# Kernel tuning notes

Measured on AMD Instinct MI355X. Metric: run time of the kernel, lower is better.

The kernel has to match this reference:

```python
import jax, jax.numpy as jnp
import numpy as np

T, N, F_IND, F_MAC = 250, 4000, 46, 178
H = 64
F_IN = F_IND + F_MAC  # dense-net input = firm chars + tiled macro = 224


def setup_inputs() -> dict:
    key = jax.random.key(0)
    ks = jax.random.split(key, 9)
    macro_features = jax.random.normal(ks[0], (1, T, F_MAC), jnp.float32)
    individual_features = jax.random.normal(ks[1], (1, T, N, F_IND), jnp.float32)
    masks = jnp.ones((1, T, N, 1), dtype=bool)
    returns_tensor = jax.random.normal(ks[2], (1, T, N, 1), jnp.float32) * 0.05
    W1 = jax.random.normal(ks[3], (F_IN, H), jnp.float32) / np.sqrt(F_IN).astype(np.float32)
    b1 = jnp.zeros((H,), jnp.float32)
    W2 = jax.random.normal(ks[4], (H, H), jnp.float32) / np.sqrt(H).astype(np.float32)
    b2 = jnp.zeros((H,), jnp.float32)
    W3 = jax.random.normal(ks[5], (H, 1), jnp.float32) / np.sqrt(H).astype(np.float32)
    b3 = jnp.zeros((1,), jnp.float32)
    return {"macro_features": macro_features, "individual_features": individual_features,
            "masks": masks, "returns_tensor": returns_tensor,
            "W1": W1, "b1": b1, "W2": W2, "b2": b2, "W3": W3, "b3": b3}


def reference(macro_features, individual_features, masks, returns_tensor, W1, b1, W2, b2, W3, b3):
    B, Tt, Nn, _ = individual_features.shape
    # tile macro state over assets and concat with firm characteristics -> [1,T,N,F_IN]
    mac = jnp.broadcast_to(macro_features[:, :, None, :], (B, Tt, Nn, macro_features.shape[-1]))
    dense_inputs = jnp.concatenate([individual_features, mac], axis=-1)
    mf = masks.astype(dense_inputs.dtype)  # [1,T,N,1]
    # dense net: 2 relu hidden layers + linear head, output_size=1 (SDF weight per firm-month)
    h = jax.nn.relu(dense_inputs @ W1 + b1)
    h = jax.nn.relu(h @ W2 + b2)
    weights = (h @ W3 + b3) * mf  # zero out masked entries (mask is all-ones -> static shape)
    # weighted returns and per-time segment sum (== torch.split + per-segment torch.sum)
    weighted_returns = returns_tensor * weights * mf
    num_val_per_time = jnp.sum(mf[0, :, :, 0], axis=1)  # [T]
    sum_per_time = jnp.sum(weighted_returns[0, :, :, 0], axis=1)  # [T]
    # normalize_w = True
    sum_per_time = sum_per_time / num_val_per_time * jnp.mean(num_val_per_time)
    sdf = (sum_per_time + 1.0)[:, None]  # [T,1]
    weights_flat = weights.reshape(1, Tt * Nn, 1)  # matches masked_select layout (all-true mask)
    return sdf, weights_flat
```

## Files before the change

kernel.cpp:

```cpp
#include <hip/hip_runtime.h>

#define T_DIM 250
#define N_DIM 4000
#define F_IND 46
#define F_MAC 178
#define H_DIM 64

typedef __bf16         bf16x8  __attribute__((ext_vector_type(8)));
typedef float          f32x4   __attribute__((ext_vector_type(4)));
typedef unsigned short ushort8 __attribute__((ext_vector_type(8)));
typedef float          f32x4a8 __attribute__((ext_vector_type(4), aligned(8)));

union FragU { ushort8 u; bf16x8 b; };
union BF2   { unsigned u; __bf16 h[2]; };

__device__ __forceinline__ unsigned short f2bf(float f) {
    unsigned u = __float_as_uint(f);
    return (unsigned short)((u + 0x7fffu + ((u >> 16) & 1u)) >> 16);
}
__device__ __forceinline__ unsigned packbf2(float lo, float hi) {
    BF2 p; p.h[0] = (__bf16)lo; p.h[1] = (__bf16)hi; return p.u;
}

__global__ __launch_bounds__(256)
void prep_kernel(const float* __restrict__ mac,
                 const float* __restrict__ W1,
                 const float* __restrict__ b1,
                 const float* __restrict__ W2,
                 unsigned short* __restrict__ Wb1,
                 unsigned short* __restrict__ Wb2,
                 float* __restrict__ Mproj,
                 float* __restrict__ sdf)
{
    const int b = blockIdx.x;
    const int tid = threadIdx.x;
    if (b < 2) {
        const float* W = (b == 0) ? W1 : W2;
        unsigned short* dst = (b == 0) ? Wb1 : Wb2;
        const int kmax = (b == 0) ? F_IND : H_DIM;
        for (int idx = tid; idx < 4096; idx += 256) {
            int j  = idx & 7;
            int L  = (idx >> 3) & 63;
            int rt = (idx >> 9) & 3;
            int s  = idx >> 11;
            int k  = s * 32 + ((L >> 4) * 8) + j;
            int c  = rt * 16 + (L & 15);
            float v = (k < kmax) ? W[k * H_DIM + c] : 0.0f;
            dst[idx] = f2bf(v);
        }
    } else {
        __shared__ float red[4][H_DIM];
        const int t  = b - 2;
        const int j  = tid & 63;
        const int kc = tid >> 6;
        const int k0 = kc * 45;
        const int k1 = (k0 + 45 < F_MAC) ? k0 + 45 : F_MAC;
        float acc = (kc == 0) ? b1[j] : 0.0f;
        const float* mrow = mac + t * F_MAC;
        for (int k = k0; k < k1; ++k)
            acc = fmaf(mrow[k], W1[(F_IND + k) * H_DIM + j], acc);
        red[kc][j] = acc;
        __syncthreads();
        if (tid < 64) {
            Mproj[t * H_DIM + j] = red[0][j] + red[1][j] + red[2][j] + red[3][j];
            if (tid == 0) sdf[t] = 1.0f;
        }
    }
}

__global__ __launch_bounds__(256, 3)
void mlp_mfma(const float* __restrict__ ind,
              const float* __restrict__ ret,
              const unsigned short* __restrict__ Wb1,
              const unsigned short* __restrict__ Wb2,
              const float* __restrict__ Mproj,
              const float* __restrict__ b2,
              const float* __restrict__ W3,
              const float* __restrict__ b3,
              float* __restrict__ out_w,
              float* __restrict__ sdf)
{
    __shared__ unsigned Hsh[256 * 32];

    const int tid  = threadIdx.x;
    const int lane = tid & 63;
    const int w    = tid >> 6;
    const int q    = lane >> 4;
    const int m    = lane & 15;
    const int m7   = m & 7;
    const int t    = blockIdx.y;
    const int n0   = blockIdx.x * 256;
    const int rbase = w * 64;
    const int nwave = n0 + rbase;

    const int  nlane = nwave + lane;
    const bool lval  = nlane < N_DIM;
    float retv = 0.0f;
    if (lval) retv = ret[(size_t)t * N_DIM + nlane];

    const float* xr = ind + ((size_t)t * N_DIM + (nwave + m)) * F_IND;
    const int CTS = 16 * F_IND;
    const bool fullw = (nwave + 64 <= N_DIM);

    const f32x4a8 z4 = {};

    f32x4a8 xa[4], xb[4];
    if (fullw) {
        #pragma unroll
        for (int ct = 0; ct < 4; ++ct) {
            const float* p = xr + ct * CTS + q * 8;
            xa[ct] = *(const f32x4a8*)(p);
            xb[ct] = *(const f32x4a8*)(p + 4);
        }
    } else {
        #pragma unroll
        for (int ct = 0; ct < 4; ++ct) {
            const float* p = xr + ct * CTS + q * 8;
            if ((nwave + ct * 16 + m) < N_DIM) {
                xa[ct] = *(const f32x4a8*)(p);
                xb[ct] = *(const f32x4a8*)(p + 4);
            } else { xa[ct] = z4; xb[ct] = z4; }
        }
    }

    FragU a1s0[4];
    #pragma unroll
    for (int rt = 0; rt < 4; ++rt)
        a1s0[rt].u = *(const ushort8*)(Wb1 + (rt * 64 + lane) * 8);
    f32x4 mp[4];
    #pragma unroll
    for (int rt = 0; rt < 4; ++rt)
        mp[rt] = *(const f32x4*)(Mproj + t * H_DIM + rt * 16 + q * 4);

    FragU xf[4];
    #pragma unroll
    for (int ct = 0; ct < 4; ++ct)
        #pragma unroll
        for (int i = 0; i < 4; ++i) {
            xf[ct].b[i]     = (__bf16)xa[ct][i];
            xf[ct].b[i + 4] = (__bf16)xb[ct][i];
        }

    f32x4a8 ya[4] = {}, yb[4] = {};
    if (q == 0) {
        #pragma unroll
        for (int ct = 0; ct < 4; ++ct)
            if (fullw || (nwave + ct * 16 + m) < N_DIM) {
                ya[ct] = *(const f32x4a8*)(xr + ct * CTS + 32);
                yb[ct] = *(const f32x4a8*)(xr + ct * CTS + 36);
            }
    } else if (q == 1) {
        #pragma unroll
        for (int ct = 0; ct < 4; ++ct)
            if (fullw || (nwave + ct * 16 + m) < N_DIM) {
                ya[ct] = *(const f32x4a8*)(xr + ct * CTS + 40);
                float2 z = *(const float2*)(xr + ct * CTS + 44);
                yb[ct][0] = z.x; yb[ct][1] = z.y;
            }
    }

    f32x4 acc[4][4];
    #pragma unroll
    for (int rt = 0; rt < 4; ++rt)
        #pragma unroll
        for (int ct = 0; ct < 4; ++ct)
            acc[rt][ct] = mp[rt];

    #pragma unroll
    for (int rt = 0; rt < 4; ++rt)
        #pragma unroll
        for (int ct = 0; ct < 4; ++ct)
            acc[rt][ct] = __builtin_amdgcn_mfma_f32_16x16x32_bf16(
                a1s0[rt].b, xf[ct].b, acc[rt][ct], 0, 0, 0);

    FragU a1s1[4];
    #pragma unroll
    for (int rt = 0; rt < 4; ++rt)
        a1s1[rt].u = *(const ushort8*)(Wb1 + ((4 + rt) * 64 + lane) * 8);

    FragU yf[4];
    #pragma unroll
    for (int ct = 0; ct < 4; ++ct)
        #pragma unroll
        for (int i = 0; i < 4; ++i) {
            yf[ct].b[i]     = (__bf16)ya[ct][i];
            yf[ct].b[i + 4] = (__bf16)yb[ct][i];
        }

    #pragma unroll
    for (int rt = 0; rt < 4; ++rt)
        #pragma unroll
        for (int ct = 0; ct < 4; ++ct)
            acc[rt][ct] = __builtin_amdgcn_mfma_f32_16x16x32_bf16(
                a1s1[rt].b, yf[ct].b, acc[rt][ct], 0, 0, 0);

    FragU a2[2][4];
    #pragma unroll
    for (int s = 0; s < 2; ++s)
        #pragma unroll
        for (int rt = 0; rt < 4; ++rt)
            a2[s][rt].u = *(const ushort8*)(Wb2 + ((s * 4 + rt) * 64 + lane) * 8);
    f32x4 bb2[4];
    #pragma unroll
    for (int rt = 0; rt < 4; ++rt)
        bb2[rt] = *(const f32x4*)(b2 + rt * 16 + q * 4);

    #pragma unroll
    for (int rt = 0; rt < 4; ++rt)
        #pragma unroll
        for (int ct = 0; ct < 4; ++ct) {
            int sl = ct * 16 + m;
            unsigned lo = packbf2(fmaxf(acc[rt][ct][0], 0.0f),
                                  fmaxf(acc[rt][ct][1], 0.0f));
            unsigned hi = packbf2(fmaxf(acc[rt][ct][2], 0.0f),
                                  fmaxf(acc[rt][ct][3], 0.0f));
            int phys = ((rt * 2 + (q >> 1)) ^ m7) * 4 + (q & 1) * 2;
            uint2 v; v.x = lo; v.y = hi;
            *(uint2*)(Hsh + (rbase + sl) * 32 + phys) = v;
        }

    #pragma unroll
    for (int rt = 0; rt < 4; ++rt)
        #pragma unroll
        for (int ct = 0; ct < 4; ++ct)
            acc[rt][ct] = bb2[rt];

    #pragma unroll
    for (int s = 0; s < 2; ++s) {
        FragU hf[4];
        #pragma unroll
        for (int ct = 0; ct < 4; ++ct) {
            int sl  = ct * 16 + m;
            int blk = (s * 4 + q) ^ m7;
            hf[ct].u = *(const ushort8*)(Hsh + (rbase + sl) * 32 + blk * 4);
        }
        #pragma unroll
        for (int rt = 0; rt < 4; ++rt)
            #pragma unroll
            for (int ct = 0; ct < 4; ++ct)
                acc[rt][ct] = __builtin_amdgcn_mfma_f32_16x16x32_bf16(
                    a2[s][rt].b, hf[ct].b, acc[rt][ct], 0, 0, 0);
    }

    float wv;
    {
        f32x4 w3[4];
        #pragma unroll
        for (int rt = 0; rt < 4; ++rt)
            w3[rt] = *(const f32x4*)(W3 + rt * 16 + q * 4);
        const float b3s = b3[0];

        float pq[4];
        #pragma unroll
        for (int ct = 0; ct < 4; ++ct) {
            float p = 0.0f;
            #pragma unroll
            for (int rt = 0; rt < 4; ++rt)
                #pragma unroll
                for (int r = 0; r < 4; ++r)
                    p = fmaf(fmaxf(acc[rt][ct][r], 0.0f), w3[rt][r], p);
            p += __shfl_xor(p, 16, 64);
            p += __shfl_xor(p, 32, 64);
            pq[ct] = p;
        }
        wv = (q == 0) ? pq[0] : (q == 1) ? pq[1] : (q == 2) ? pq[2] : pq[3];
        wv += b3s;
    }

    float contrib = 0.0f;
    if (lval) {
        out_w[(size_t)t * N_DIM + nlane] = wv;
        contrib = retv * wv;
    }
    #pragma unroll
    for (int off = 32; off > 0; off >>= 1)
        contrib += __shfl_down(contrib, off, 64);
    if (lane == 0) atomicAdd(&sdf[t], contrib);
}

extern "C" void kernel_launch(void* const* d_in, const int* in_sizes, int n_in,
                              void* d_out, int out_size, void* d_ws, size_t ws_size,
                              hipStream_t stream) {
    (void)in_sizes; (void)n_in; (void)out_size; (void)ws_size;

    const float* mac = (const float*)d_in[0];
    const float* ind = (const float*)d_in[1];
    const float* ret = (const float*)d_in[3];
    const float* W1  = (const float*)d_in[4];
    const float* b1  = (const float*)d_in[5];
    const float* W2  = (const float*)d_in[6];
    const float* b2  = (const float*)d_in[7];
    const float* W3  = (const float*)d_in[8];
    const float* b3  = (const float*)d_in[9];

    float* sdf   = (float*)d_out;
    float* out_w = (float*)d_out + T_DIM;

    unsigned short* Wb1 = (unsigned short*)d_ws;
    unsigned short* Wb2 = Wb1 + 4096;
    float* Mproj = (float*)((char*)d_ws + 16384);

    prep_kernel<<<dim3(252), 256, 0, stream>>>(mac, W1, b1, W2, Wb1, Wb2, Mproj, sdf);

    dim3 grid((N_DIM + 255) / 256, T_DIM);
    mlp_mfma<<<grid, 256, 0, stream>>>(ind, ret, Wb1, Wb2, Mproj, b2, W3, b3,
                                       out_w, sdf);
}
```

Before: 321.6 us.

## Make MLP blocks persistent over 8 row tiles with software-prefetched inputs

```diff
diff --git a/kernel.cpp b/kernel.cpp
--- a/kernel.cpp
+++ b/kernel.cpp
@@ -11,7 +11,7 @@
 typedef unsigned short ushort8 __attribute__((ext_vector_type(8)));
 typedef float          f32x4a8 __attribute__((ext_vector_type(4), aligned(8)));
 
-union FragU { ushort8 u; bf16x8 b; };
+union FragU { ushort8 u; bf16x8 b; unsigned w[4]; };
 union BF2   { unsigned u; __bf16 h[2]; };
 
 __device__ __forceinline__ unsigned short f2bf(float f) {
@@ -68,7 +68,7 @@
     }
 }
 
-__global__ __launch_bounds__(256, 3)
+__global__ __launch_bounds__(256)
 void mlp_mfma(const float* __restrict__ ind,
               const float* __restrict__ ret,
               const unsigned short* __restrict__ Wb1,
@@ -89,166 +89,160 @@
     const int m    = lane & 15;
     const int m7   = m & 7;
     const int t    = blockIdx.y;
-    const int n0   = blockIdx.x * 256;
-    const int rbase = w * 64;
-    const int nwave = n0 + rbase;
-
-    const int  nlane = nwave + lane;
-    const bool lval  = nlane < N_DIM;
-    float retv = 0.0f;
-    if (lval) retv = ret[(size_t)t * N_DIM + nlane];
-
-    const float* xr = ind + ((size_t)t * N_DIM + (nwave + m)) * F_IND;
-    const int CTS = 16 * F_IND;
-    const bool fullw = (nwave + 64 <= N_DIM);
-
-    const f32x4a8 z4 = {};
-
-    f32x4a8 xa[4], xb[4];
-    if (fullw) {
-        #pragma unroll
-        for (int ct = 0; ct < 4; ++ct) {
-            const float* p = xr + ct * CTS + q * 8;
-            xa[ct] = *(const f32x4a8*)(p);
-            xb[ct] = *(const f32x4a8*)(p + 4);
-        }
-    } else {
-        #pragma unroll
-        for (int ct = 0; ct < 4; ++ct) {
-            const float* p = xr + ct * CTS + q * 8;
-            if ((nwave + ct * 16 + m) < N_DIM) {
-                xa[ct] = *(const f32x4a8*)(p);
-                xb[ct] = *(const f32x4a8*)(p + 4);
-            } else { xa[ct] = z4; xb[ct] = z4; }
-        }
-    }
-
-    FragU a1s0[4];
+    const int nbase = blockIdx.x * 2048;
+    const int w64  = w * 64;
+    const int rbase = w64;
+
+    FragU a1[8];
     #pragma unroll
-    for (int rt = 0; rt < 4; ++rt)
-        a1s0[rt].u = *(const ushort8*)(Wb1 + (rt * 64 + lane) * 8);
+    for (int f = 0; f < 8; ++f)
+        a1[f].u = *(const ushort8*)(Wb1 + (f * 64 + lane) * 8);
     f32x4 mp[4];
     #pragma unroll
     for (int rt = 0; rt < 4; ++rt)
         mp[rt] = *(const f32x4*)(Mproj + t * H_DIM + rt * 16 + q * 4);
 
-    FragU xf[4];
-    #pragma unroll
-    for (int ct = 0; ct < 4; ++ct)
-        #pragma unroll
-        for (int i = 0; i < 4; ++i) {
-            xf[ct].b[i]     = (__bf16)xa[ct][i];
-            xf[ct].b[i + 4] = (__bf16)xb[ct][i];
-        }
-
-    f32x4a8 ya[4] = {}, yb[4] = {};
-    if (q == 0) {
+    const float* xrw = ind + ((size_t)t * N_DIM + nbase + w64 + m) * F_IND;
+    const float* rp  = ret + (size_t)t * N_DIM + nbase + w64 + lane;
+    const int CTS = 16 * F_IND;
+
+    f32x4a8 xa[4], xb[4], ya[4], yb[4];
+    float retv;
+    const f32x4a8 z4 = {};
+
+    auto issue = [&](int ni) {
+        const float* xr = xrw + (size_t)ni * (256 * F_IND);
+        const int nwv = nbase + ni * 256 + w64;
+        const bool fullw = (nwv + 64 <= N_DIM);
+        if (fullw) {
+            #pragma unroll
+            for (int ct = 0; ct < 4; ++ct) {
+                const float* p = xr + ct * CTS + q * 8;
+                xa[ct] = *(const f32x4a8*)(p);
+                xb[ct] = *(const f32x4a8*)(p + 4);
+            }
+        } else {
+            #pragma unroll
+            for (int ct = 0; ct < 4; ++ct) {
+                const float* p = xr + ct * CTS + q * 8;
+                if ((nwv + ct * 16 + m) < N_DIM) {
+                    xa[ct] = *(const f32x4a8*)(p);
+                    xb[ct] = *(const f32x4a8*)(p + 4);
+                } else { xa[ct] = z4; xb[ct] = z4; }
+            }
+        }
+        #pragma unroll
+        for (int ct = 0; ct < 4; ++ct) { ya[ct] = z4; yb[ct] = z4; }
+        if (q == 0) {
+            #pragma unroll
+            for (int ct = 0; ct < 4; ++ct)
+                if (fullw || (nwv + ct * 16 + m) < N_DIM) {
+                    ya[ct] = *(const f32x4a8*)(xr + ct * CTS + 32);
+                    yb[ct] = *(const f32x4a8*)(xr + ct * CTS + 36);
+                }
+        } else if (q == 1) {
+            #pragma unroll
+            for (int ct = 0; ct < 4; ++ct)
+                if (fullw || (nwv + ct * 16 + m) < N_DIM) {
+                    ya[ct] = *(const f32x4a8*)(xr + ct * CTS + 40);
+                    float2 z = *(const float2*)(xr + ct * CTS + 44);
+                    yb[ct][0] = z.x; yb[ct][1] = z.y;
+                }
+        }
+        retv = 0.0f;
+        if (nwv + lane < N_DIM) retv = rp[ni * 256];
+    };
+
+    issue(0);
+
+    #pragma unroll 1
+    for (int ni = 0; ni < 8; ++ni) {
+        FragU xf[4], yf[4];
         #pragma unroll
         for (int ct = 0; ct < 4; ++ct)
-            if (fullw || (nwave + ct * 16 + m) < N_DIM) {
-                ya[ct] = *(const f32x4a8*)(xr + ct * CTS + 32);
-                yb[ct] = *(const f32x4a8*)(xr + ct * CTS + 36);
-            }
-    } else if (q == 1) {
-        #pragma unroll
-        for (int ct = 0; ct < 4; ++ct)
-            if (fullw || (nwave + ct * 16 + m) < N_DIM) {
-                ya[ct] = *(const f32x4a8*)(xr + ct * CTS + 40);
-                float2 z = *(const float2*)(xr + ct * CTS + 44);
-                yb[ct][0] = z.x; yb[ct][1] = z.y;
-            }
-    }
-
-    f32x4 acc[4][4];
-    #pragma unroll
-    for (int rt = 0; rt < 4; ++rt)
-        #pragma unroll
-        for (int ct = 0; ct < 4; ++ct)
-            acc[rt][ct] = mp[rt];
-
-    #pragma unroll
-    for (int rt = 0; rt < 4; ++rt)
-        #pragma unroll
-        for (int ct = 0; ct < 4; ++ct)
-            acc[rt][ct] = __builtin_amdgcn_mfma_f32_16x16x32_bf16(
-                a1s0[rt].b, xf[ct].b, acc[rt][ct], 0, 0, 0);
-
-    FragU a1s1[4];
-    #pragma unroll
-    for (int rt = 0; rt < 4; ++rt)
-        a1s1[rt].u = *(const ushort8*)(Wb1 + ((4 + rt) * 64 + lane) * 8);
-
-    FragU yf[4];
-    #pragma unroll
-    for (int ct = 0; ct < 4; ++ct)
-        #pragma unroll
-        for (int i = 0; i < 4; ++i) {
-            yf[ct].b[i]     = (__bf16)ya[ct][i];
-            yf[ct].b[i + 4] = (__bf16)yb[ct][i];
-        }
-
-    #pragma unroll
-    for (int rt = 0; rt < 4; ++rt)
-        #pragma unroll
-        for (int ct = 0; ct < 4; ++ct)
-            acc[rt][ct] = __builtin_amdgcn_mfma_f32_16x16x32_bf16(
-                a1s1[rt].b, yf[ct].b, acc[rt][ct], 0, 0, 0);
-
-    FragU a2[2][4];
-    #pragma unroll
-    for (int s = 0; s < 2; ++s)
-        #pragma unroll
-        for (int rt = 0; rt < 4; ++rt)
-            a2[s][rt].u = *(const ushort8*)(Wb2 + ((s * 4 + rt) * 64 + lane) * 8);
-    f32x4 bb2[4];
-    #pragma unroll
-    for (int rt = 0; rt < 4; ++rt)
-        bb2[rt] = *(const f32x4*)(b2 + rt * 16 + q * 4);
-
-    #pragma unroll
-    for (int rt = 0; rt < 4; ++rt)
-        #pragma unroll
-        for (int ct = 0; ct < 4; ++ct) {
-            int sl = ct * 16 + m;
-            unsigned lo = packbf2(fmaxf(acc[rt][ct][0], 0.0f),
-                                  fmaxf(acc[rt][ct][1], 0.0f));
-            unsigned hi = packbf2(fmaxf(acc[rt][ct][2], 0.0f),
-                                  fmaxf(acc[rt][ct][3], 0.0f));
-            int phys = ((rt * 2 + (q >> 1)) ^ m7) * 4 + (q & 1) * 2;
-            uint2 v; v.x = lo; v.y = hi;
-            *(uint2*)(Hsh + (rbase + sl) * 32 + phys) = v;
-        }
-
-    #pragma unroll
-    for (int rt = 0; rt < 4; ++rt)
-        #pragma unroll
-        for (int ct = 0; ct < 4; ++ct)
-            acc[rt][ct] = bb2[rt];
-
-    #pragma unroll
-    for (int s = 0; s < 2; ++s) {
-        FragU hf[4];
-        #pragma unroll
-        for (int ct = 0; ct < 4; ++ct) {
-            int sl  = ct * 16 + m;
-            int blk = (s * 4 + q) ^ m7;
-            hf[ct].u = *(const ushort8*)(Hsh + (rbase + sl) * 32 + blk * 4);
-        }
+            #pragma unroll
+            for (int i = 0; i < 4; ++i) {
+                xf[ct].b[i]     = (__bf16)xa[ct][i];
+                xf[ct].b[i + 4] = (__bf16)xb[ct][i];
+                yf[ct].b[i]     = (__bf16)ya[ct][i];
+                yf[ct].b[i + 4] = (__bf16)yb[ct][i];
+            }
+        const float retc = retv;
+        const int nwv   = nbase + ni * 256 + w64;
+        const int nlane = nwv + lane;
+
+        if (ni < 7) issue(ni + 1);
+
+        f32x4 acc[4][4];
+        #pragma unroll
+        for (int rt = 0; rt < 4; ++rt)
+            #pragma unroll
+            for (int ct = 0; ct < 4; ++ct)
+                acc[rt][ct] = mp[rt];
+
         #pragma unroll
         for (int rt = 0; rt < 4; ++rt)
             #pragma unroll
             for (int ct = 0; ct < 4; ++ct)
                 acc[rt][ct] = __builtin_amdgcn_mfma_f32_16x16x32_bf16(
-                    a2[s][rt].b, hf[ct].b, acc[rt][ct], 0, 0, 0);
-    }
-
-    float wv;
-    {
-        f32x4 w3[4];
-        #pragma unroll
-        for (int rt = 0; rt < 4; ++rt)
-            w3[rt] = *(const f32x4*)(W3 + rt * 16 + q * 4);
+                    a1[rt].b, xf[ct].b, acc[rt][ct], 0, 0, 0);
+        #pragma unroll
+        for (int rt = 0; rt < 4; ++rt)
+            #pragma unroll
+            for (int ct = 0; ct < 4; ++ct)
+                acc[rt][ct] = __builtin_amdgcn_mfma_f32_16x16x32_bf16(
+                    a1[4 + rt].b, yf[ct].b, acc[rt][ct], 0, 0, 0);
+
+        FragU a2[2][4];
+        #pragma unroll
+        for (int s = 0; s < 2; ++s)
+            #pragma unroll
+            for (int rt = 0; rt < 4; ++rt)
+                a2[s][rt].u = *(const ushort8*)(Wb2 + ((s * 4 + rt) * 64 + lane) * 8);
+        f32x4 bb2[4], w3[4];
+        #pragma unroll
+        for (int rt = 0; rt < 4; ++rt) {
+            bb2[rt] = *(const f32x4*)(b2 + rt * 16 + q * 4);
+            w3[rt]  = *(const f32x4*)(W3 + rt * 16 + q * 4);
+        }
         const float b3s = b3[0];
+
+        #pragma unroll
+        for (int rt = 0; rt < 4; ++rt)
+            #pragma unroll
+            for (int ct = 0; ct < 4; ++ct) {
+                int sl = ct * 16 + m;
+                unsigned lo = packbf2(fmaxf(acc[rt][ct][0], 0.0f),
+                                      fmaxf(acc[rt][ct][1], 0.0f));
+                unsigned hi = packbf2(fmaxf(acc[rt][ct][2], 0.0f),
+                                      fmaxf(acc[rt][ct][3], 0.0f));
+                int phys = ((rt * 2 + (q >> 1)) ^ m7) * 4 + (q & 1) * 2;
+                uint2 v; v.x = lo; v.y = hi;
+                *(uint2*)(Hsh + (rbase + sl) * 32 + phys) = v;
+            }
+
+        #pragma unroll
+        for (int rt = 0; rt < 4; ++rt)
+            #pragma unroll
+            for (int ct = 0; ct < 4; ++ct)
+                acc[rt][ct] = bb2[rt];
+
+        #pragma unroll
+        for (int s = 0; s < 2; ++s) {
+            FragU hf[4];
+            #pragma unroll
+            for (int ct = 0; ct < 4; ++ct) {
+                int sl  = ct * 16 + m;
+                int blk = (s * 4 + q) ^ m7;
+                hf[ct].u = *(const ushort8*)(Hsh + (rbase + sl) * 32 + blk * 4);
+            }
+            #pragma unroll
+            for (int rt = 0; rt < 4; ++rt)
+                #pragma unroll
+                for (int ct = 0; ct < 4; ++ct)
+                    acc[rt][ct] = __builtin_amdgcn_mfma_f32_16x16x32_bf16(
+                        a2[s][rt].b, hf[ct].b, acc[rt][ct], 0, 0, 0);
+        }
 
         float pq[4];
         #pragma unroll
@@ -263,19 +257,19 @@
             p += __shfl_xor(p, 32, 64);
             pq[ct] = p;
         }
-        wv = (q == 0) ? pq[0] : (q == 1) ? pq[1] : (q == 2) ? pq[2] : pq[3];
+        float wv = (q == 0) ? pq[0] : (q == 1) ? pq[1] : (q == 2) ? pq[2] : pq[3];
         wv += b3s;
+
+        float contrib = 0.0f;
+        if (nlane < N_DIM) {
+            out_w[(size_t)t * N_DIM + nlane] = wv;
+            contrib = retc * wv;
+        }
+        #pragma unroll
+        for (int off = 32; off > 0; off >>= 1)
+            contrib += __shfl_down(contrib, off, 64);
+        if (lane == 0) atomicAdd(&sdf[t], contrib);
     }
-
-    float contrib = 0.0f;
-    if (lval) {
-        out_w[(size_t)t * N_DIM + nlane] = wv;
-        contrib = retv * wv;
-    }
-    #pragma unroll
-    for (int off = 32; off > 0; off >>= 1)
-        contrib += __shfl_down(contrib, off, 64);
-    if (lane == 0) atomicAdd(&sdf[t], contrib);
 }
 
 extern "C" void kernel_launch(void* const* d_in, const int* in_sizes, int n_in,
@@ -302,7 +296,7 @@
 
     prep_kernel<<<dim3(252), 256, 0, stream>>>(mac, W1, b1, W2, Wb1, Wb2, Mproj, sdf);
 
-    dim3 grid((N_DIM + 255) / 256, T_DIM);
+    dim3 grid(2, T_DIM);
     mlp_mfma<<<grid, 256, 0, stream>>>(ind, ret, Wb1, Wb2, Mproj, b2, W3, b3,
                                        out_w, sdf);
 }
```

Measured after the change: 311.4 us. 3.2% less time.
